# Kernel tuning notes

Measured on AMD Instinct MI355X. Metric: run time of the kernel, lower is better.

## Reference

```python
import jax, jax.numpy as jnp
import numpy as np


def setup_inputs() -> dict:
    key = jax.random.key(0)
    k1, k2, k3 = jax.random.split(key, 3)
    vol_shape = (4, 1, 128, 192, 192)   # [B, C, D, H, W]
    dsc_shape = (4, 1, 8, 12, 12)       # PatchGAN-style discriminator logits
    return {
        "dsc_fake": jax.random.normal(k1, dsc_shape, dtype=jnp.float32),
        "predicts": jax.random.normal(k2, vol_shape, dtype=jnp.float32),
        "y_data": jax.random.normal(k3, vol_shape, dtype=jnp.float32),
        "zeros": jnp.zeros(dsc_shape, dtype=jnp.float32),
    }


def reference(dsc_fake, predicts, y_data, zeros):
    # BCE with logits (stable form), target = zeros
    bce = jnp.mean(
        jnp.maximum(dsc_fake, 0.0) - dsc_fake * zeros
        + jnp.log1p(jnp.exp(-jnp.abs(dsc_fake)))
    )
    # L1 loss between target volume and prediction
    g_loss_l1 = jnp.mean(jnp.abs(y_data - predicts))
    # Finite-difference gradient MSE along D, H, W (axes 2,3,4).
    # Original detaches to numpy, so this term carries no gradient.
    yd = jax.lax.stop_gradient(y_data)
    pr = jax.lax.stop_gradient(predicts)
    g_loss_gd = jnp.float32(0.0)
    for ax in (2, 3, 4):
        gy = jnp.abs(jnp.gradient(yd, axis=ax))   # central diff interior, one-sided edges
        gp = jnp.abs(jnp.gradient(pr, axis=ax))
        g_loss_gd = g_loss_gd + jnp.mean((gy - gp) ** 2)
    return bce + 100.0 * g_loss_l1 + 100.0 * g_loss_gd
```

## Files before the change

kernel.cpp:

```cpp
#include <hip/hip_runtime.h>
#include <math.h>

namespace {
constexpr int BATCH = 4;
constexpr int DDIM  = 128;
constexpr int HDIM  = 192;
constexpr int WDIM  = 192;
constexpr long long NTOT = (long long)BATCH * DDIM * HDIM * WDIM;
constexpr int GW   = WDIM / 4;
constexpr int HS4  = GW;
constexpr int DS4  = GW * HDIM;
constexpr int NDSC = 4 * 1 * 8 * 12 * 12;
constexpr int BLOCK = 256;
constexpr int DC    = 16;
constexpr int NCH   = DDIM / DC;
constexpr int NCOL  = BATCH * HDIM * GW;
constexpr int NTHREADS = NCOL * NCH;
constexpr int GRID  = NTHREADS / BLOCK;
}

__device__ __forceinline__ float4 ld4(const float* __restrict__ p, long long g) {
    return *(const float4*)(p + 4LL * g);
}

__global__ __launch_bounds__(BLOCK, 4) void vol_kernel(const float* __restrict__ p,
                                                       const float* __restrict__ y,
                                                       float* __restrict__ acc) {
    const int t   = blockIdx.x * BLOCK + threadIdx.x;
    const int gw  = t % GW;
    int rest      = t / GW;
    const int h   = rest % HDIM; rest /= HDIM;
    const int b   = rest % BATCH;
    const int chunk = rest / BATCH;
    const int d0  = chunk * DC;

    const int   hmo = (h > 0)        ? HS4 : 0;
    const int   hpo = (h < HDIM - 1) ? HS4 : 0;
    const float sh  = (h == 0 || h == HDIM - 1) ? 1.f : 0.5f;
    const int   wlo = (gw > 0)       ? -1 : 0;
    const int   wro = (gw < GW - 1)  ? 4 : 3;
    const float swx = (gw == 0)      ? 1.f : 0.5f;
    const float sww = (gw == GW - 1) ? 1.f : 0.5f;

    long long g = (((long long)b * DDIM + d0) * HDIM + h) * GW + gw;

    const long long gm = g - ((d0 > 0) ? DS4 : 0);
    float4 ym = ld4(y, gm), pm = ld4(p, gm);
    float4 yc = ld4(y, g),  pc = ld4(p, g);

    float l1 = 0.f, gd = 0.f;

    #pragma unroll 4
    for (int i = 0; i < DC; ++i) {
        const int d = d0 + i;
        const long long gn = g + ((d < DDIM - 1) ? DS4 : 0);
        const float4 yn = ld4(y, gn);
        const float4 pn = ld4(p, gn);
        const float sd = (d == 0 || d == DDIM - 1) ? 1.f : 0.5f;

        const float4 yhm = ld4(y, g - hmo), yhp = ld4(y, g + hpo);
        const float4 phm = ld4(p, g - hmo), php = ld4(p, g + hpo);

        const float* yr = y + 4LL * g;
        const float* pr = p + 4LL * g;
        const float ywl = yr[wlo], ywr = yr[wro];
        const float pwl = pr[wlo], pwr = pr[wro];

        l1 += fabsf(yc.x - pc.x) + fabsf(yc.y - pc.y)
            + fabsf(yc.z - pc.z) + fabsf(yc.w - pc.w);

        float t0, gy, gp;
        gy = (yc.y - ywl) * swx;  gp = (pc.y - pwl) * swx;
        t0 = fabsf(gy) - fabsf(gp); gd += t0 * t0;
        gy = (yc.z - yc.x) * 0.5f; gp = (pc.z - pc.x) * 0.5f;
        t0 = fabsf(gy) - fabsf(gp); gd += t0 * t0;
        gy = (yc.w - yc.y) * 0.5f; gp = (pc.w - pc.y) * 0.5f;
        t0 = fabsf(gy) - fabsf(gp); gd += t0 * t0;
        gy = (ywr - yc.z) * sww;  gp = (pwr - pc.z) * sww;
        t0 = fabsf(gy) - fabsf(gp); gd += t0 * t0;

        t0 = fabsf((yhp.x - yhm.x) * sh) - fabsf((php.x - phm.x) * sh); gd += t0 * t0;
        t0 = fabsf((yhp.y - yhm.y) * sh) - fabsf((php.y - phm.y) * sh); gd += t0 * t0;
        t0 = fabsf((yhp.z - yhm.z) * sh) - fabsf((php.z - phm.z) * sh); gd += t0 * t0;
        t0 = fabsf((yhp.w - yhm.w) * sh) - fabsf((php.w - phm.w) * sh); gd += t0 * t0;

        t0 = fabsf((yn.x - ym.x) * sd) - fabsf((pn.x - pm.x) * sd); gd += t0 * t0;
        t0 = fabsf((yn.y - ym.y) * sd) - fabsf((pn.y - pm.y) * sd); gd += t0 * t0;
        t0 = fabsf((yn.z - ym.z) * sd) - fabsf((pn.z - pm.z) * sd); gd += t0 * t0;
        t0 = fabsf((yn.w - ym.w) * sd) - fabsf((pn.w - pm.w) * sd); gd += t0 * t0;

        ym = yc; yc = yn; pm = pc; pc = pn; g = gn;
    }

    __shared__ float lds1[4], lds2[4];
    #pragma unroll
    for (int off = 32; off > 0; off >>= 1) {
        l1 += __shfl_down(l1, off, 64);
        gd += __shfl_down(gd, off, 64);
    }
    const int lane = threadIdx.x & 63;
    const int wave = threadIdx.x >> 6;
    if (lane == 0) { lds1[wave] = l1; lds2[wave] = gd; }
    __syncthreads();
    if (threadIdx.x == 0) {
        atomicAdd(&acc[0], lds1[0] + lds1[1] + lds1[2] + lds1[3]);
        atomicAdd(&acc[1], lds2[0] + lds2[1] + lds2[2] + lds2[3]);
    }
}

__global__ __launch_bounds__(BLOCK) void finalize_kernel(const float* __restrict__ dsc,
                                                         const float* __restrict__ acc,
                                                         float* __restrict__ out) {
    float s = 0.f;
    for (int i = threadIdx.x; i < NDSC; i += BLOCK) {
        const float x = dsc[i];
        s += fmaxf(x, 0.f) + log1pf(expf(-fabsf(x)));
    }
    __shared__ float lds[4];
    #pragma unroll
    for (int off = 32; off > 0; off >>= 1)
        s += __shfl_down(s, off, 64);
    if ((threadIdx.x & 63) == 0) lds[threadIdx.x >> 6] = s;
    __syncthreads();
    if (threadIdx.x == 0) {
        const float bce = (lds[0] + lds[1] + lds[2] + lds[3]) / (float)NDSC;
        const float l1m = acc[0] / (float)NTOT;
        const float gdm = acc[1] / (float)NTOT;
        out[0] = bce + 100.f * (l1m + gdm);
    }
}

extern "C" void kernel_launch(void* const* d_in, const int* in_sizes, int n_in,
                              void* d_out, int out_size, void* d_ws, size_t ws_size,
                              hipStream_t stream) {
    const float* dsc_fake = (const float*)d_in[0];
    const float* predicts = (const float*)d_in[1];
    const float* y_data   = (const float*)d_in[2];
    float* acc = (float*)d_ws;
    float* out = (float*)d_out;

    hipMemsetAsync(d_ws, 0, 2 * sizeof(float), stream);
    vol_kernel<<<GRID, BLOCK, 0, stream>>>(predicts, y_data, acc);
    finalize_kernel<<<1, BLOCK, 0, stream>>>(dsc_fake, acc, out);
}
```

Before: 217.3 us.

## Prefetch next D-slice loads and replace atomics with per-block partial sums

Restructures the D-marching loop to issue the next slice's neighbour loads one iteration ahead so memory latency overlaps with arithmetic, and halves the D chunk per thread to launch more threads. Removes the memset and global atomics by writing per-block partials that the finalize kernel reduces. Costs extra registers for the prefetched values and more redundant halo loads from shorter chunks.

```diff
diff --git a/kernel.cpp b/kernel.cpp
--- a/kernel.cpp
+++ b/kernel.cpp
@@ -12,7 +12,7 @@
 constexpr int DS4  = GW * HDIM;
 constexpr int NDSC = 4 * 1 * 8 * 12 * 12;
 constexpr int BLOCK = 256;
-constexpr int DC    = 16;
+constexpr int DC    = 8;
 constexpr int NCH   = DDIM / DC;
 constexpr int NCOL  = BATCH * HDIM * GW;
 constexpr int NTHREADS = NCOL * NCH;
@@ -23,16 +23,15 @@
     return *(const float4*)(p + 4LL * g);
 }
 
-__global__ __launch_bounds__(BLOCK, 4) void vol_kernel(const float* __restrict__ p,
-                                                       const float* __restrict__ y,
-                                                       float* __restrict__ acc) {
+__global__ __launch_bounds__(BLOCK) void vol_kernel(const float* __restrict__ p,
+                                                    const float* __restrict__ y,
+                                                    float* __restrict__ part) {
     const int t   = blockIdx.x * BLOCK + threadIdx.x;
     const int gw  = t % GW;
     int rest      = t / GW;
     const int h   = rest % HDIM; rest /= HDIM;
     const int b   = rest % BATCH;
-    const int chunk = rest / BATCH;
-    const int d0  = chunk * DC;
+    const int d0  = (rest / BATCH) * DC;
 
     const int   hmo = (h > 0)        ? HS4 : 0;
     const int   hpo = (h < HDIM - 1) ? HS4 : 0;
@@ -47,24 +46,32 @@
     const long long gm = g - ((d0 > 0) ? DS4 : 0);
     float4 ym = ld4(y, gm), pm = ld4(p, gm);
     float4 yc = ld4(y, g),  pc = ld4(p, g);
+    long long gn = g + DS4;
+    float4 yn = ld4(y, gn), pn = ld4(p, gn);
+    float4 yhm = ld4(y, g - hmo), yhp = ld4(y, g + hpo);
+    float4 phm = ld4(p, g - hmo), php = ld4(p, g + hpo);
+    float ywl = y[4LL * g + wlo], ywr = y[4LL * g + wro];
+    float pwl = p[4LL * g + wlo], pwr = p[4LL * g + wro];
 
     float l1 = 0.f, gd = 0.f;
 
-    #pragma unroll 4
+    #pragma unroll
     for (int i = 0; i < DC; ++i) {
         const int d = d0 + i;
-        const long long gn = g + ((d < DDIM - 1) ? DS4 : 0);
-        const float4 yn = ld4(y, gn);
-        const float4 pn = ld4(p, gn);
+
+        float4 ynn, pnn, yhm2, yhp2, phm2, php2;
+        float ywl2, ywr2, pwl2, pwr2;
+        long long gnn = gn;
+        if (i < DC - 1) {
+            gnn = gn + ((d + 2 < DDIM) ? DS4 : 0);
+            ynn  = ld4(y, gnn);      pnn  = ld4(p, gnn);
+            yhm2 = ld4(y, gn - hmo); yhp2 = ld4(y, gn + hpo);
+            phm2 = ld4(p, gn - hmo); php2 = ld4(p, gn + hpo);
+            ywl2 = y[4LL * gn + wlo]; ywr2 = y[4LL * gn + wro];
+            pwl2 = p[4LL * gn + wlo]; pwr2 = p[4LL * gn + wro];
+        }
+
         const float sd = (d == 0 || d == DDIM - 1) ? 1.f : 0.5f;
-
-        const float4 yhm = ld4(y, g - hmo), yhp = ld4(y, g + hpo);
-        const float4 phm = ld4(p, g - hmo), php = ld4(p, g + hpo);
-
-        const float* yr = y + 4LL * g;
-        const float* pr = p + 4LL * g;
-        const float ywl = yr[wlo], ywr = yr[wro];
-        const float pwl = pr[wlo], pwr = pr[wro];
 
         l1 += fabsf(yc.x - pc.x) + fabsf(yc.y - pc.y)
             + fabsf(yc.z - pc.z) + fabsf(yc.w - pc.w);
@@ -89,7 +96,13 @@
         t0 = fabsf((yn.z - ym.z) * sd) - fabsf((pn.z - pm.z) * sd); gd += t0 * t0;
         t0 = fabsf((yn.w - ym.w) * sd) - fabsf((pn.w - pm.w) * sd); gd += t0 * t0;
 
-        ym = yc; yc = yn; pm = pc; pc = pn; g = gn;
+        if (i < DC - 1) {
+            ym = yc; yc = yn; yn = ynn;
+            pm = pc; pc = pn; pn = pnn;
+            yhm = yhm2; yhp = yhp2; phm = phm2; php = php2;
+            ywl = ywl2; ywr = ywr2; pwl = pwl2; pwr = pwr2;
+            g = gn; gn = gnn;
+        }
     }
 
     __shared__ float lds1[4], lds2[4];
@@ -98,34 +111,45 @@
         l1 += __shfl_down(l1, off, 64);
         gd += __shfl_down(gd, off, 64);
     }
-    const int lane = threadIdx.x & 63;
-    const int wave = threadIdx.x >> 6;
-    if (lane == 0) { lds1[wave] = l1; lds2[wave] = gd; }
+    if ((threadIdx.x & 63) == 0) {
+        lds1[threadIdx.x >> 6] = l1;
+        lds2[threadIdx.x >> 6] = gd;
+    }
     __syncthreads();
     if (threadIdx.x == 0) {
-        atomicAdd(&acc[0], lds1[0] + lds1[1] + lds1[2] + lds1[3]);
-        atomicAdd(&acc[1], lds2[0] + lds2[1] + lds2[2] + lds2[3]);
+        part[2 * blockIdx.x]     = lds1[0] + lds1[1] + lds1[2] + lds1[3];
+        part[2 * blockIdx.x + 1] = lds2[0] + lds2[1] + lds2[2] + lds2[3];
     }
 }
 
 __global__ __launch_bounds__(BLOCK) void finalize_kernel(const float* __restrict__ dsc,
-                                                         const float* __restrict__ acc,
+                                                         const float* __restrict__ part,
                                                          float* __restrict__ out) {
-    float s = 0.f;
+    float l1 = 0.f, gd = 0.f, s = 0.f;
+    for (int i = threadIdx.x; i < GRID; i += BLOCK) {
+        l1 += part[2 * i];
+        gd += part[2 * i + 1];
+    }
     for (int i = threadIdx.x; i < NDSC; i += BLOCK) {
         const float x = dsc[i];
         s += fmaxf(x, 0.f) + log1pf(expf(-fabsf(x)));
     }
-    __shared__ float lds[4];
+    __shared__ float a[4], c[4], e[4];
     #pragma unroll
-    for (int off = 32; off > 0; off >>= 1)
-        s += __shfl_down(s, off, 64);
-    if ((threadIdx.x & 63) == 0) lds[threadIdx.x >> 6] = s;
+    for (int off = 32; off > 0; off >>= 1) {
+        l1 += __shfl_down(l1, off, 64);
+        gd += __shfl_down(gd, off, 64);
+        s  += __shfl_down(s,  off, 64);
+    }
+    if ((threadIdx.x & 63) == 0) {
+        const int w = threadIdx.x >> 6;
+        a[w] = l1; c[w] = gd; e[w] = s;
+    }
     __syncthreads();
     if (threadIdx.x == 0) {
-        const float bce = (lds[0] + lds[1] + lds[2] + lds[3]) / (float)NDSC;
-        const float l1m = acc[0] / (float)NTOT;
-        const float gdm = acc[1] / (float)NTOT;
+        const float bce = (e[0] + e[1] + e[2] + e[3]) / (float)NDSC;
+        const float l1m = (a[0] + a[1] + a[2] + a[3]) / (float)NTOT;
+        const float gdm = (c[0] + c[1] + c[2] + c[3]) / (float)NTOT;
         out[0] = bce + 100.f * (l1m + gdm);
     }
 }
@@ -136,10 +160,9 @@
     const float* dsc_fake = (const float*)d_in[0];
     const float* predicts = (const float*)d_in[1];
     const float* y_data   = (const float*)d_in[2];
-    float* acc = (float*)d_ws;
-    float* out = (float*)d_out;
+    float* part = (float*)d_ws;
+    float* out  = (float*)d_out;
 
-    hipMemsetAsync(d_ws, 0, 2 * sizeof(float), stream);
-    vol_kernel<<<GRID, BLOCK, 0, stream>>>(predicts, y_data, acc);
-    finalize_kernel<<<1, BLOCK, 0, stream>>>(dsc_fake, acc, out);
+    vol_kernel<<<GRID, BLOCK, 0, stream>>>(predicts, y_data, part);
+    finalize_kernel<<<1, BLOCK, 0, stream>>>(dsc_fake, part, out);
 }
```

Measured after the change: 192.4 us. 1.13x faster.
